# Kernel optimization log

Measured on AMD Instinct MI355X. Metric: run time of the kernel, lower is better.

The kernel has to match this reference:

```python
import jax, jax.numpy as jnp
import numpy as np

B, N_IN, L, W, N_OUT, D = 4096, 1024, 8, 1024, 1024, 16
W_SCALE = 0.25  # 1/sqrt(fan_in) so tanh does not saturate


def setup_inputs() -> dict:
    key = jax.random.key(0)
    ks = jax.random.split(key, 5)
    x = jax.random.normal(ks[0], (B, N_IN), dtype=jnp.float32)
    # each hidden-layer node gathers D values from the previous layer
    src_hidden = jax.random.randint(ks[1], (L, W, D), 0, N_IN, dtype=jnp.int32)
    w_hidden = jax.random.normal(ks[2], (L, W, D), dtype=jnp.float32) * W_SCALE
    src_out = jax.random.randint(ks[3], (N_OUT, D), 0, W, dtype=jnp.int32)
    w_out = jax.random.normal(ks[4], (N_OUT, D), dtype=jnp.float32) * W_SCALE
    return {"x": x, "src_hidden": src_hidden, "w_hidden": w_hidden,
            "src_out": src_out, "w_out": w_out}


def reference(x, src_hidden, w_hidden, src_out, w_out):
    # Topological-order evaluation, one fused gather-weighted-sum-activation
    # per layer instead of the original per-node Python loop.
    def layer(vals, sw):
        src, w = sw                                   # [W, D] each
        # vals[:, src]: [B, W, D] gather; weighted incoming sum then tanh
        new_vals = jnp.tanh(jnp.sum(vals[:, src] * w, axis=-1))  # [B, W]
        return new_vals, None

    vals, _ = jax.lax.scan(layer, x, (src_hidden, w_hidden))
    # output nodes: identity activation (weighted sum only)
    out = jnp.sum(vals[:, src_out] * w_out, axis=-1)   # [B, N_OUT]
    return out
```

## Files before the change

### kernel.cpp

```cpp
#include <hip/hip_runtime.h>


#define TB       16
#define W_NODES  1024
#define LAYERS   8
#define ROW_H    16
#define BUF_H    (W_NODES * ROW_H)

typedef _Float16 h8 __attribute__((ext_vector_type(8)));

__device__ __forceinline__ float fast_tanh(float x) {
    float a = __builtin_amdgcn_exp2f(x * 2.8853900817779268f);
    return 1.0f - 2.0f * __builtin_amdgcn_rcpf(a + 1.0f);
}

__global__ __launch_bounds__(1024) void genome_net(
    const float* __restrict__ x,
    const int*   __restrict__ src_hidden,
    const float* __restrict__ w_hidden,
    const int*   __restrict__ src_out,
    const float* __restrict__ w_out,
    float*       __restrict__ out)
{
    extern __shared__ _Float16 lds[];
    _Float16* bufA = lds;
    _Float16* bufB = lds + BUF_H;

    const int tid  = threadIdx.x;
    const int wave = tid >> 6;
    const int lane = tid & 63;
    const int nsub = lane & 31;
    const int ch   = lane >> 5;
    const int b0   = blockIdx.x * TB;

    #pragma unroll
    for (int r = 0; r < 2; ++r) {
        const int n = (r << 9) + (wave << 5) + nsub;
        h8 hv;
        #pragma unroll
        for (int j = 0; j < 8; ++j)
            hv[j] = (_Float16)x[(size_t)(b0 + (ch << 3) + j) * W_NODES + n];
        *(h8*)(bufA + n * ROW_H + (ch << 3)) = hv;
    }
    __syncthreads();

    _Float16* rd = bufA;
    _Float16* wr = bufB;

    #pragma unroll 1
    for (int l = 0; l < LAYERS; ++l) {
        #pragma unroll 1
        for (int r = 0; r < 2; ++r) {
            const int n   = (r << 9) + (wave << 5) + nsub;
            const int row = (l << 10) + n;
            const int4*   sp = (const int4*)(src_hidden) + (row << 2);
            const float4* wp = (const float4*)(w_hidden) + (row << 2);
            int4   s4[4]; float4 w4[4];
            #pragma unroll
            for (int q = 0; q < 4; ++q) { s4[q] = sp[q]; w4[q] = wp[q]; }
            int   s_arr[16]; float w_arr[16];
            #pragma unroll
            for (int q = 0; q < 4; ++q) {
                s_arr[4*q+0] = s4[q].x; s_arr[4*q+1] = s4[q].y;
                s_arr[4*q+2] = s4[q].z; s_arr[4*q+3] = s4[q].w;
                w_arr[4*q+0] = w4[q].x; w_arr[4*q+1] = w4[q].y;
                w_arr[4*q+2] = w4[q].z; w_arr[4*q+3] = w4[q].w;
            }

            float acc[8];
            #pragma unroll
            for (int j = 0; j < 8; ++j) acc[j] = 0.0f;

            #pragma unroll
            for (int d = 0; d < 16; ++d) {
                const h8 v = *(const h8*)(rd + (s_arr[d] << 4) + (ch << 3));
                const float w = w_arr[d];
                #pragma unroll
                for (int j = 0; j < 8; ++j)
                    acc[j] = fmaf((float)v[j], w, acc[j]);
            }

            h8 hv;
            #pragma unroll
            for (int j = 0; j < 8; ++j) hv[j] = (_Float16)fast_tanh(acc[j]);
            *(h8*)(wr + n * ROW_H + (ch << 3)) = hv;
        }
        __syncthreads();
        _Float16* tmp = rd; rd = wr; wr = tmp;
    }

    #pragma unroll 1
    for (int r = 0; r < 2; ++r) {
        const int n = (r << 9) + (wave << 5) + nsub;
        const int4*   sp = (const int4*)(src_out) + (n << 2);
        const float4* wp = (const float4*)(w_out) + (n << 2);
        int4   s4[4]; float4 w4[4];
        #pragma unroll
        for (int q = 0; q < 4; ++q) { s4[q] = sp[q]; w4[q] = wp[q]; }
        int   s_arr[16]; float w_arr[16];
        #pragma unroll
        for (int q = 0; q < 4; ++q) {
            s_arr[4*q+0] = s4[q].x; s_arr[4*q+1] = s4[q].y;
            s_arr[4*q+2] = s4[q].z; s_arr[4*q+3] = s4[q].w;
            w_arr[4*q+0] = w4[q].x; w_arr[4*q+1] = w4[q].y;
            w_arr[4*q+2] = w4[q].z; w_arr[4*q+3] = w4[q].w;
        }

        float acc[8];
        #pragma unroll
        for (int j = 0; j < 8; ++j) acc[j] = 0.0f;

        #pragma unroll
        for (int d = 0; d < 16; ++d) {
            const h8 v = *(const h8*)(rd + (s_arr[d] << 4) + (ch << 3));
            const float w = w_arr[d];
            #pragma unroll
            for (int j = 0; j < 8; ++j)
                acc[j] = fmaf((float)v[j], w, acc[j]);
        }

        #pragma unroll
        for (int j = 0; j < 8; ++j)
            out[(size_t)(b0 + (ch << 3) + j) * W_NODES + n] = acc[j];
    }
}

extern "C" void kernel_launch(void* const* d_in, const int* in_sizes, int n_in,
                              void* d_out, int out_size, void* d_ws, size_t ws_size,
                              hipStream_t stream) {
    const float* x  = (const float*)d_in[0];
    const int*   sh = (const int*)  d_in[1];
    const float* wh = (const float*)d_in[2];
    const int*   so = (const int*)  d_in[3];
    const float* wo = (const float*)d_in[4];
    float* out = (float*)d_out;

    const int shmem = 2 * BUF_H * (int)sizeof(_Float16);
    hipFuncSetAttribute(reinterpret_cast<const void*>(genome_net),
                        hipFuncAttributeMaxDynamicSharedMemorySize, shmem);

    genome_net<<<dim3(4096 / TB), dim3(1024), shmem, stream>>>(x, sh, wh, so, wo, out);
}
```

Before: 116.7 us.

## Permute gather slots per row to spread LDS bank accesses across lanes

Adds a preprocessing kernel that reorders each node's 16 (src, weight) pairs. Pairs are grouped by src modulo 4, and each slot d is assigned a group that rotates with the node index, so neighbouring lanes tend to hit different LDS bank groups when they gather in the same iteration. The aim is fewer bank conflicts in the random LDS gathers of the main kernel. In exchange it adds two extra kernel launches per call, uses workspace memory, and changes the floating-point summation order.

Result: slower. 142.9 us (+22.5%).

```diff
diff --git a/kernel.cpp b/kernel.cpp
--- a/kernel.cpp
+++ b/kernel.cpp
@@ -12,6 +12,37 @@
 __device__ __forceinline__ float fast_tanh(float x) {
     float a = __builtin_amdgcn_exp2f(x * 2.8853900817779268f);
     return 1.0f - 2.0f * __builtin_amdgcn_rcpf(a + 1.0f);
+}
+
+__global__ __launch_bounds__(256) void permute_rows(
+    const int* __restrict__ src, const float* __restrict__ w,
+    int* __restrict__ ps, float* __restrict__ pw, int nrows)
+{
+    const int rid = blockIdx.x * blockDim.x + threadIdx.x;
+    if (rid >= nrows) return;
+    const int n    = rid & 1023;
+    const int base = rid << 4;
+
+    int   s[16]; float wt[16];
+    #pragma unroll
+    for (int d = 0; d < 16; ++d) { s[d] = src[base + d]; wt[d] = w[base + d]; }
+
+    int cnt[4] = {0, 0, 0, 0};
+    int lst[4][16];
+    for (int d = 0; d < 16; ++d) { const int g = s[d] & 3; lst[g][cnt[g]++] = d; }
+
+    for (int slot = 0; slot < 16; ++slot) {
+        int g = (slot + n) & 3;
+        if (cnt[g] == 0) {
+            g = 0;
+            if (cnt[1] > cnt[g]) g = 1;
+            if (cnt[2] > cnt[g]) g = 2;
+            if (cnt[3] > cnt[g]) g = 3;
+        }
+        const int e = lst[g][--cnt[g]];
+        ps[base + slot] = s[e];
+        pw[base + slot] = wt[e];
+    }
 }
 
 __global__ __launch_bounds__(1024) void genome_net(
@@ -135,9 +166,29 @@
     const float* wo = (const float*)d_in[4];
     float* out = (float*)d_out;
 
+    const size_t HID = (size_t)LAYERS * W_NODES * 16;
+    const size_t OUT = (size_t)W_NODES * 16;
+    const size_t need = (HID + OUT) * 8;
+
+    const int*   sh_use = sh; const float* wh_use = wh;
+    const int*   so_use = so; const float* wo_use = wo;
+
+    if (ws_size >= need) {
+        int*   ps_h = (int*)d_ws;
+        float* pw_h = (float*)((char*)d_ws + HID * 4);
+        int*   ps_o = (int*)((char*)d_ws + HID * 8);
+        float* pw_o = (float*)((char*)d_ws + HID * 8 + OUT * 4);
+        permute_rows<<<dim3((LAYERS * W_NODES + 255) / 256), dim3(256), 0, stream>>>(
+            sh, wh, ps_h, pw_h, LAYERS * W_NODES);
+        permute_rows<<<dim3((W_NODES + 255) / 256), dim3(256), 0, stream>>>(
+            so, wo, ps_o, pw_o, W_NODES);
+        sh_use = ps_h; wh_use = pw_h; so_use = ps_o; wo_use = pw_o;
+    }
+
     const int shmem = 2 * BUF_H * (int)sizeof(_Float16);
     hipFuncSetAttribute(reinterpret_cast<const void*>(genome_net),
                         hipFuncAttributeMaxDynamicSharedMemorySize, shmem);
 
-    genome_net<<<dim3(4096 / TB), dim3(1024), shmem, stream>>>(x, sh, wh, so, wo, out);
+    genome_net<<<dim3(4096 / TB), dim3(1024), shmem, stream>>>(
+        x, sh_use, wh_use, so_use, wo_use, out);
 }
```
